# Optimization experiments

Measured on AMD Instinct MI355X. Metric: run time of the kernel, lower is better.

Reference implementation:

```python
import jax, jax.numpy as jnp
import numpy as np

V, E, H, A = 10000, 512, 512, 512  # vocab, embed, hidden, att_odim (== enc dim)
B, T_ENC, L = 32, 1500, 100
BOS, EOS = 1, 2
ATT_H = 512  # attention MLP hidden dim


def setup_inputs() -> dict:
    key = jax.random.key(0)
    ks = jax.random.split(key, 12)
    s = 0.02
    enc_pad = jax.random.normal(ks[0], (B, T_ENC, A), dtype=jnp.float32)
    enc_len = jax.random.randint(ks[1], (B,), T_ENC // 2, T_ENC + 1)
    ys = jax.random.randint(ks[2], (B, L), 3, V)
    return {
        "enc_pad": enc_pad,
        "enc_len": enc_len,
        "ys": ys,
        "emb_table": jax.random.normal(ks[3], (V, E), jnp.float32) * s,
        "W_ih": jax.random.normal(ks[4], (4 * H, E + A), jnp.float32) * s,
        "W_hh": jax.random.normal(ks[5], (4 * H, H), jnp.float32) * s,
        "b_ih": jnp.zeros((4 * H,), jnp.float32),
        "b_hh": jnp.zeros((4 * H,), jnp.float32),
        "W_enc": jax.random.normal(ks[6], (A, ATT_H), jnp.float32) * s,
        "W_dec": jax.random.normal(ks[7], (H, ATT_H), jnp.float32) * s,
        "v_att": jax.random.normal(ks[8], (ATT_H,), jnp.float32) * s,
        "W_out": jax.random.normal(ks[9], (V, H + A), jnp.float32) * s,
        "b_out": jnp.zeros((V,), jnp.float32),
    }


def reference(enc_pad, enc_len, ys, emb_table, W_ih, W_hh, b_ih, b_hh,
              W_enc, W_dec, v_att, W_out, b_out):
    # Teacher-forced decoder (tf_rate=1.0, dropout=0, eval mode, no label smoothing)
    Bz = enc_pad.shape[0]
    bos_col = jnp.full((Bz, 1), BOS, dtype=ys.dtype)
    eos_col = jnp.full((Bz, 1), EOS, dtype=ys.dtype)
    ys_in = jnp.concatenate([bos_col, ys], axis=1)    # [B, L+1]
    ys_out = jnp.concatenate([ys, eos_col], axis=1)   # [B, L+1]
    eys = emb_table[ys_in]                            # [B, L+1, E]

    mask = jnp.arange(enc_pad.shape[1])[None, :] < enc_len[:, None]  # [B, T]
    enc_proj = jnp.einsum('btd,da->bta', enc_pad, W_enc)             # precompute once

    dec_z0 = jnp.zeros((Bz, W_hh.shape[1]), enc_pad.dtype)
    dec_c0 = jnp.zeros((Bz, W_hh.shape[1]), enc_pad.dtype)
    c0 = jnp.zeros((Bz, enc_pad.shape[2]), enc_pad.dtype)

    def step(carry, emb_t):
        dec_z, dec_c, c = carry
        cell_inp = jnp.concatenate([emb_t, c], axis=-1)          # [B, E+A]
        gates = cell_inp @ W_ih.T + b_ih + dec_z @ W_hh.T + b_hh  # [B, 4H]
        i_g, f_g, g_g, o_g = jnp.split(gates, 4, axis=-1)
        dec_c = jax.nn.sigmoid(f_g) * dec_c + jax.nn.sigmoid(i_g) * jnp.tanh(g_g)
        dec_z = jax.nn.sigmoid(o_g) * jnp.tanh(dec_c)
        # additive attention over encoder states, masked by enc_len
        e = jnp.tanh(enc_proj + (dec_z @ W_dec)[:, None, :]) @ v_att  # [B, T]
        e = jnp.where(mask, e, jnp.float32(-1e9))
        w = jax.nn.softmax(e, axis=-1)                                # [B, T]
        c = jnp.einsum('bt,btd->bd', w, enc_pad)                      # [B, A]
        logit = jnp.concatenate([dec_z, c], axis=-1) @ W_out.T + b_out
        return (dec_z, dec_c, c), (logit, w)

    _, (logits_t, ws_t) = jax.lax.scan(step, (dec_z0, dec_c0, c0),
                                       jnp.swapaxes(eys, 0, 1))
    logits = jnp.swapaxes(logits_t, 0, 1)   # [B, L+1, V]
    ws = jnp.swapaxes(ws_t, 0, 1)           # [B, L+1, T]

    log_probs = jax.nn.log_softmax(logits, axis=2)
    prediction = jnp.argmax(logits, axis=-1)
    ys_log_probs = jnp.take_along_axis(log_probs, ys_out[:, :, None], axis=2)[:, :, 0]
    return logits, ys_log_probs, prediction, ws
```

## Files before the change

### kernel.cpp

```cpp
#include <hip/hip_runtime.h>
#include <math.h>

#define BZ   32
#define TENC 1500
#define DD   512
#define VV   10000
#define LL   100
#define SS   101
#define G4   2048
#define KCZ  1024
#define ACH  32
#define NCH  47

#define OUT_LOGITS 0
#define OUT_ENCP   0
#define OUT_PREG   24576000
#define OUT_YSLP   32320000
#define OUT_PRED   32323232
#define OUT_WS     32326464

#define WS_ZA      0
#define WS_CST     3342336
#define WS_LALL    3358720
#define WS_Q       3361952
#define WS_ZERON   3361952

__device__ inline float sigm(float x) { return 1.f / (1.f + __expf(-x)); }
__device__ inline float tanh_fast(float x) {
    x = fminf(15.f, fmaxf(-15.f, x));
    float e = __expf(2.f * x);
    return (e - 1.f) / (e + 1.f);
}

__global__ void zero_kernel(float* ws) {
    size_t i = (size_t)blockIdx.x * 256 + threadIdx.x;
    if (i < WS_ZERON) ws[i] = 0.f;
}

template<int MODE>
__global__ __launch_bounds__(256) void gemm_tile(
    const float* __restrict__ Abase, const float* __restrict__ Bmat,
    const float* __restrict__ bias0, const float* __restrict__ bias1,
    const int* __restrict__ ys, const float* __restrict__ l_all,
    float* __restrict__ Out, int M, int N, int K)
{
    __shared__ float As[16][132];
    __shared__ float Bs[16][132];
    const int tid = threadIdx.x;
    const int row0 = blockIdx.y * 128, n0 = blockIdx.x * 128;

    const int ar = tid >> 1, ah = tid & 1;
    int am = row0 + ar; if (am > M - 1) am = M - 1;
    const float* Arow;
    float linvA = 1.f;
    if (MODE == 0) {
        Arow = Abase + (size_t)am * 512;
    } else if (MODE == 1) {
        int t = am >> 5, b = am & 31;
        int tok = (t == 0) ? 1 : ys[b * LL + t - 1];
        Arow = Abase + (size_t)tok * 512;
    } else {
        Arow = Abase + (size_t)(am + 32) * 1024;
        linvA = 1.f / l_all[am];
    }
    const int bk = tid >> 4, bg = tid & 15;
    const int bn = tid >> 1, bh = tid & 1;
    int bnn = n0 + bn; if (bnn > N - 1) bnn = N - 1;

    const int tx = tid & 15, ty = tid >> 4;
    const int rr = ty * 8, cc = tx * 8;
    float acc[8][8] = {{0.f}};

    for (int k0 = 0; k0 < K; k0 += 16) {
        float4 a0 = *(const float4*)(Arow + k0 + ah * 8);
        float4 a1 = *(const float4*)(Arow + k0 + ah * 8 + 4);
        if (MODE == 2) {
            float sc = (k0 + ah * 8 >= 512) ? linvA : 1.f;
            a0.x *= sc; a0.y *= sc; a0.z *= sc; a0.w *= sc;
            a1.x *= sc; a1.y *= sc; a1.z *= sc; a1.w *= sc;
        }
        As[ah*8+0][ar] = a0.x; As[ah*8+1][ar] = a0.y; As[ah*8+2][ar] = a0.z; As[ah*8+3][ar] = a0.w;
        As[ah*8+4][ar] = a1.x; As[ah*8+5][ar] = a1.y; As[ah*8+6][ar] = a1.z; As[ah*8+7][ar] = a1.w;
        if (MODE == 0) {
            const float* bp = Bmat + (size_t)(k0 + bk) * N + n0 + bg * 8;
            float4 b0 = *(const float4*)(bp);
            float4 b1 = *(const float4*)(bp + 4);
            *(float4*)&Bs[bk][bg * 8]     = b0;
            *(float4*)&Bs[bk][bg * 8 + 4] = b1;
        } else {
            const float* bp = Bmat + (size_t)bnn * 1024 + k0 + bh * 8;
            float4 b0 = *(const float4*)(bp);
            float4 b1 = *(const float4*)(bp + 4);
            Bs[bh*8+0][bn] = b0.x; Bs[bh*8+1][bn] = b0.y; Bs[bh*8+2][bn] = b0.z; Bs[bh*8+3][bn] = b0.w;
            Bs[bh*8+4][bn] = b1.x; Bs[bh*8+5][bn] = b1.y; Bs[bh*8+6][bn] = b1.z; Bs[bh*8+7][bn] = b1.w;
        }
        __syncthreads();
        #pragma unroll
        for (int kk = 0; kk < 16; ++kk) {
            float4 A0 = *(const float4*)&As[kk][rr];
            float4 A1 = *(const float4*)&As[kk][rr + 4];
            float4 B0 = *(const float4*)&Bs[kk][cc];
            float4 B1 = *(const float4*)&Bs[kk][cc + 4];
            float av[8] = {A0.x, A0.y, A0.z, A0.w, A1.x, A1.y, A1.z, A1.w};
            float bv[8] = {B0.x, B0.y, B0.z, B0.w, B1.x, B1.y, B1.z, B1.w};
            #pragma unroll
            for (int i = 0; i < 8; ++i)
                #pragma unroll
                for (int j = 0; j < 8; ++j)
                    acc[i][j] += av[i] * bv[j];
        }
        __syncthreads();
    }
    #pragma unroll
    for (int i = 0; i < 8; ++i) {
        int m = row0 + rr + i;
        if (m >= M) continue;
        size_t orow;
        if (MODE == 2) { int t = m >> 5, b = m & 31; orow = ((size_t)b * SS + t) * (size_t)N; }
        else orow = (size_t)m * N;
        #pragma unroll
        for (int j = 0; j < 8; ++j) {
            int n = n0 + cc + j;
            if (n < N) {
                float v = acc[i][j];
                if (MODE == 1) v += bias0[n] + bias1[n];
                if (MODE == 2) v += bias0[n];
                Out[orow + n] = v;
            }
        }
    }
}

__global__ __launch_bounds__(512) void k_glstm(
    const float* __restrict__ za_t, const float* __restrict__ pre_g_t,
    const float* __restrict__ W_ih, const float* __restrict__ W_hh,
    const float* __restrict__ l_all, int t,
    float* __restrict__ c_state, float* __restrict__ za_n)
{
    __shared__ float red[128];
    const int h = blockIdx.x, tid = threadIdx.x;
    const int wave = tid >> 6, lane = tid & 63;
    const int gl = wave & 3, bh = wave >> 2;
    const int r = gl * 512 + h;
    const float* wz = W_hh + (size_t)r * 512;
    const float* wc = W_ih + (size_t)r * 1024 + 512;
    const float4 wz0 = *(const float4*)(wz + lane * 4);
    const float4 wz1 = *(const float4*)(wz + 256 + lane * 4);
    const float4 wc0 = *(const float4*)(wc + lane * 4);
    const float4 wc1 = *(const float4*)(wc + 256 + lane * 4);

    #pragma unroll 2
    for (int i = 0; i < 16; ++i) {
        const int b = bh * 16 + i;
        const float* zr = za_t + b * KCZ;
        float4 z0 = *(const float4*)(zr + lane * 4);
        float4 z1 = *(const float4*)(zr + 256 + lane * 4);
        float4 c0 = *(const float4*)(zr + 512 + lane * 4);
        float4 c1 = *(const float4*)(zr + 768 + lane * 4);
        float az = z0.x*wz0.x + z0.y*wz0.y + z0.z*wz0.z + z0.w*wz0.w
                 + z1.x*wz1.x + z1.y*wz1.y + z1.z*wz1.z + z1.w*wz1.w;
        float ac = c0.x*wc0.x + c0.y*wc0.y + c0.z*wc0.z + c0.w*wc0.w
                 + c1.x*wc1.x + c1.y*wc1.y + c1.z*wc1.z + c1.w*wc1.w;
        float linv = (t == 0) ? 0.f : 1.f / l_all[(t - 1) * 32 + b];
        float v = az + ac * linv;
        #pragma unroll
        for (int off = 32; off > 0; off >>= 1) v += __shfl_xor(v, off);
        if (lane == 0) red[gl * 32 + b] = v;
    }
    __syncthreads();
    if (tid < 32) {
        const int bb = tid;
        const float* pg = pre_g_t + bb * G4 + h;
        float vi = red[  0 + bb] + pg[0];
        float vf = red[ 32 + bb] + pg[512];
        float vg = red[ 64 + bb] + pg[1024];
        float vo = red[ 96 + bb] + pg[1536];
        float ig = sigm(vi), fg = sigm(vf), gg = tanhf(vg), og = sigm(vo);
        float c = fg * c_state[bb * 512 + h] + ig * gg;
        c_state[bb * 512 + h] = c;
        za_n[bb * KCZ + h] = og * tanhf(c);
    }
}

__global__ __launch_bounds__(256) void k_qproj(const float* __restrict__ za_n,
                                               const float* __restrict__ W_dec,
                                               float* __restrict__ q)
{
    __shared__ float red[256];
    const int tid = threadIdx.x;
    const int j = blockIdx.x * 32 + (tid & 31);
    const int b = blockIdx.y;
    const int k0 = (tid >> 5) * 64;
    const float* z = za_n + b * KCZ + k0;
    const float* wd = W_dec + (size_t)k0 * 512 + j;
    float acc = 0.f;
    #pragma unroll 8
    for (int k = 0; k < 64; k += 4) {
        float4 z4 = *(const float4*)(z + k);
        acc += z4.x * wd[(k + 0) * 512] + z4.y * wd[(k + 1) * 512]
             + z4.z * wd[(k + 2) * 512] + z4.w * wd[(k + 3) * 512];
    }
    red[tid] = acc;
    __syncthreads();
    if (tid < 32) {
        float s = red[tid] + red[tid + 32] + red[tid + 64] + red[tid + 96]
                + red[tid + 128] + red[tid + 160] + red[tid + 192] + red[tid + 224];
        q[b * 512 + blockIdx.x * 32 + tid] = s;
    }
}

__global__ __launch_bounds__(256) void k_att(
    const float* __restrict__ enc_proj, const float* __restrict__ enc_pad,
    const float* __restrict__ q, const float* __restrict__ v_att,
    const int* __restrict__ enc_len,
    float* __restrict__ za_n, float* __restrict__ l_t, float* __restrict__ w_raw)
{
    __shared__ float q_s[512], v_s[512];
    __shared__ float accs[4][512];
    __shared__ float lsum_s[4];
    const int b = blockIdx.y, tc = blockIdx.x, tid = threadIdx.x;
    int len = enc_len[b]; if (len > TENC) len = TENC;
    const int base = tc * ACH;
    int tlim = base + ACH;
    if (tlim > len) tlim = len;
    if (base >= tlim) return;

    for (int i = tid; i < 512; i += 256) { q_s[i] = q[b * 512 + i]; v_s[i] = v_att[i]; }
    __syncthreads();
    const int wave = tid >> 6, lane = tid & 63;
    float a[8] = {0.f, 0.f, 0.f, 0.f, 0.f, 0.f, 0.f, 0.f};
    float lacc = 0.f;
    float qv[8], vv8[8];
    #pragma unroll
    for (int j = 0; j < 8; ++j) { qv[j] = q_s[lane * 8 + j]; vv8[j] = v_s[lane * 8 + j]; }

    for (int tp = base + wave; tp < tlim; tp += 4) {
        const float* ep = enc_proj + ((size_t)b * TENC + tp) * 512 + lane * 8;
        float4 e0 = *(const float4*)(ep);
        float4 e1 = *(const float4*)(ep + 4);
        float s = tanh_fast(e0.x + qv[0]) * vv8[0] + tanh_fast(e0.y + qv[1]) * vv8[1]
                + tanh_fast(e0.z + qv[2]) * vv8[2] + tanh_fast(e0.w + qv[3]) * vv8[3]
                + tanh_fast(e1.x + qv[4]) * vv8[4] + tanh_fast(e1.y + qv[5]) * vv8[5]
                + tanh_fast(e1.z + qv[6]) * vv8[6] + tanh_fast(e1.w + qv[7]) * vv8[7];
        #pragma unroll
        for (int off = 32; off > 0; off >>= 1) s += __shfl_xor(s, off);
        float p = __expf(s - 10.f);
        if (lane == 0) w_raw[(size_t)b * (SS * TENC) + tp] = p;
        lacc += p;
        const float* xp = enc_pad + ((size_t)b * TENC + tp) * 512 + lane * 8;
        float4 x0 = *(const float4*)(xp);
        float4 x1 = *(const float4*)(xp + 4);
        a[0] += p * x0.x; a[1] += p * x0.y; a[2] += p * x0.z; a[3] += p * x0.w;
        a[4] += p * x1.x; a[5] += p * x1.y; a[6] += p * x1.z; a[7] += p * x1.w;
    }
    #pragma unroll
    for (int j = 0; j < 8; ++j) accs[wave][lane * 8 + j] = a[j];
    if (lane == 0) lsum_s[wave] = lacc;
    __syncthreads();
    for (int d = tid; d < 512; d += 256) {
        float s = accs[0][d] + accs[1][d] + accs[2][d] + accs[3][d];
        atomicAdd(&za_n[b * KCZ + 512 + d], s);
    }
    if (tid == 0) atomicAdd(&l_t[b], lsum_s[0] + lsum_s[1] + lsum_s[2] + lsum_s[3]);
}

__global__ __launch_bounds__(256) void k_wnorm(float* __restrict__ wsatt,
                                               const float* __restrict__ l_all,
                                               const int* __restrict__ enc_len)
{
    const int rid = blockIdx.x;
    const int b = rid / SS, t = rid % SS;
    const float linv = 1.f / l_all[t * 32 + b];
    const int len = enc_len[b];
    float* row = wsatt + (size_t)rid * TENC;
    for (int tp = threadIdx.x; tp < TENC; tp += 256)
        row[tp] = (tp < len) ? row[tp] * linv : 0.f;
}

__global__ __launch_bounds__(256) void k_logsm(const float* __restrict__ logits,
                                               const int* __restrict__ ys,
                                               float* __restrict__ ys_lp,
                                               float* __restrict__ pred)
{
    __shared__ float sval[256];
    __shared__ int   sidx[256];
    __shared__ float ssum[256];
    const int bid = blockIdx.x, tid = threadIdx.x;
    const float* row = logits + (size_t)bid * VV;
    float vmax = -3.4e38f; int imax = 0;
    for (int v4 = tid; v4 < VV / 4; v4 += 256) {
        float4 x = *(const float4*)(row + v4 * 4);
        int basei = v4 * 4;
        if (x.x > vmax) { vmax = x.x; imax = basei; }
        if (x.y > vmax) { vmax = x.y; imax = basei + 1; }
        if (x.z > vmax) { vmax = x.z; imax = basei + 2; }
        if (x.w > vmax) { vmax = x.w; imax = basei + 3; }
    }
    sval[tid] = vmax; sidx[tid] = imax;
    __syncthreads();
    for (int s = 128; s > 0; s >>= 1) {
        if (tid < s) {
            float v2 = sval[tid + s]; int i2 = sidx[tid + s];
            if (v2 > sval[tid] || (v2 == sval[tid] && i2 < sidx[tid])) { sval[tid] = v2; sidx[tid] = i2; }
        }
        __syncthreads();
    }
    const float gmax = sval[0];
    float lsum = 0.f;
    for (int v4 = tid; v4 < VV / 4; v4 += 256) {
        float4 x = *(const float4*)(row + v4 * 4);
        lsum += __expf(x.x - gmax) + __expf(x.y - gmax) + __expf(x.z - gmax) + __expf(x.w - gmax);
    }
    ssum[tid] = lsum;
    __syncthreads();
    for (int s = 128; s > 0; s >>= 1) {
        if (tid < s) ssum[tid] += ssum[tid + s];
        __syncthreads();
    }
    if (tid == 0) {
        int b = bid / SS, t = bid % SS;
        int tok = (t < LL) ? ys[b * LL + t] : 2;
        ys_lp[bid] = row[tok] - gmax - logf(ssum[0]);
        pred[bid]  = (float)sidx[0];
    }
}

extern "C" void kernel_launch(void* const* d_in, const int* in_sizes, int n_in,
                              void* d_out, int out_size, void* d_ws, size_t ws_size,
                              hipStream_t stream)
{
    const float* enc_pad = (const float*)d_in[0];
    const int*   enc_len = (const int*)d_in[1];
    const int*   ys      = (const int*)d_in[2];
    const float* emb     = (const float*)d_in[3];
    const float* W_ih    = (const float*)d_in[4];
    const float* W_hh    = (const float*)d_in[5];
    const float* b_ih    = (const float*)d_in[6];
    const float* b_hh    = (const float*)d_in[7];
    const float* W_enc   = (const float*)d_in[8];
    const float* W_dec   = (const float*)d_in[9];
    const float* v_att   = (const float*)d_in[10];
    const float* W_out   = (const float*)d_in[11];
    const float* b_out   = (const float*)d_in[12];

    float* out = (float*)d_out;
    float* enc_proj = out + OUT_ENCP;
    float* pre_g    = out + OUT_PREG;
    float* logits   = out + OUT_LOGITS;
    float* ys_lp    = out + OUT_YSLP;
    float* predo    = out + OUT_PRED;
    float* wsatt    = out + OUT_WS;

    float* ws = (float*)d_ws;
    float* za      = ws + WS_ZA;
    float* c_state = ws + WS_CST;
    float* l_all   = ws + WS_LALL;
    float* qbuf    = ws + WS_Q;

    zero_kernel<<<(WS_ZERON + 255) / 256, 256, 0, stream>>>(ws);
    gemm_tile<0><<<dim3(4, 375), 256, 0, stream>>>(enc_pad, W_enc, nullptr, nullptr, nullptr,
                                                   nullptr, enc_proj, BZ * TENC, 512, 512);
    gemm_tile<1><<<dim3(16, 26), 256, 0, stream>>>(emb, W_ih, b_ih, b_hh, ys,
                                                   nullptr, pre_g, BZ * SS, G4, 512);

    for (int t = 0; t < SS; ++t) {
        float* za_t    = za + (size_t)t * (BZ * KCZ);
        float* za_next = za_t + BZ * KCZ;
        k_glstm<<<512, 512, 0, stream>>>(za_t, pre_g + (size_t)t * (BZ * G4),
                                         W_ih, W_hh, l_all, t, c_state, za_next);
        k_qproj<<<dim3(16, 32), 256, 0, stream>>>(za_next, W_dec, qbuf);
        k_att<<<dim3(NCH, 32), 256, 0, stream>>>(enc_proj, enc_pad, qbuf, v_att, enc_len,
                                                 za_next, l_all + t * 32,
                                                 wsatt + (size_t)t * TENC);
    }

    k_wnorm<<<BZ * SS, 256, 0, stream>>>(wsatt, l_all, enc_len);
    gemm_tile<2><<<dim3(79, 26), 256, 0, stream>>>(za, W_out, b_out, nullptr, nullptr,
                                                   l_all, logits, BZ * SS, VV, 1024);
    k_logsm<<<BZ * SS, 256, 0, stream>>>(logits, ys, ys_lp, predo);
}
```

Before: 6.261 ms.

## Store encoder projection in bf16, restructure LSTM gate matvec, single-pass log-softmax

```diff
diff --git a/kernel.cpp b/kernel.cpp
--- a/kernel.cpp
+++ b/kernel.cpp
@@ -13,7 +13,7 @@
 #define NCH  47
 
 #define OUT_LOGITS 0
-#define OUT_ENCP   0
+#define OUT_ENCPBF 0
 #define OUT_PREG   24576000
 #define OUT_YSLP   32320000
 #define OUT_PRED   32323232
@@ -31,6 +31,13 @@
     float e = __expf(2.f * x);
     return (e - 1.f) / (e + 1.f);
 }
+__device__ inline unsigned short f2bf(float x) {
+    unsigned int u = __float_as_uint(x);
+    u = (u + 0x7FFFu + ((u >> 16) & 1u)) >> 16;
+    return (unsigned short)u;
+}
+__device__ inline float bf_lo(unsigned int u) { return __uint_as_float(u << 16); }
+__device__ inline float bf_hi(unsigned int u) { return __uint_as_float(u & 0xFFFF0000u); }
 
 __global__ void zero_kernel(float* ws) {
     size_t i = (size_t)blockIdx.x * 256 + threadIdx.x;
@@ -111,21 +118,35 @@
         }
         __syncthreads();
     }
-    #pragma unroll
-    for (int i = 0; i < 8; ++i) {
-        int m = row0 + rr + i;
-        if (m >= M) continue;
-        size_t orow;
-        if (MODE == 2) { int t = m >> 5, b = m & 31; orow = ((size_t)b * SS + t) * (size_t)N; }
-        else orow = (size_t)m * N;
-        #pragma unroll
-        for (int j = 0; j < 8; ++j) {
-            int n = n0 + cc + j;
-            if (n < N) {
-                float v = acc[i][j];
-                if (MODE == 1) v += bias0[n] + bias1[n];
-                if (MODE == 2) v += bias0[n];
-                Out[orow + n] = v;
+    if (MODE == 0) {
+        unsigned short* ob = (unsigned short*)Out;
+        #pragma unroll
+        for (int i = 0; i < 8; ++i) {
+            int m = row0 + rr + i;
+            uint4 o;
+            o.x = (unsigned int)f2bf(acc[i][0]) | ((unsigned int)f2bf(acc[i][1]) << 16);
+            o.y = (unsigned int)f2bf(acc[i][2]) | ((unsigned int)f2bf(acc[i][3]) << 16);
+            o.z = (unsigned int)f2bf(acc[i][4]) | ((unsigned int)f2bf(acc[i][5]) << 16);
+            o.w = (unsigned int)f2bf(acc[i][6]) | ((unsigned int)f2bf(acc[i][7]) << 16);
+            *(uint4*)(ob + (size_t)m * 512 + n0 + cc) = o;
+        }
+    } else {
+        #pragma unroll
+        for (int i = 0; i < 8; ++i) {
+            int m = row0 + rr + i;
+            if (m >= M) continue;
+            size_t orow;
+            if (MODE == 2) { int t = m >> 5, b = m & 31; orow = ((size_t)b * SS + t) * (size_t)N; }
+            else orow = (size_t)m * N;
+            #pragma unroll
+            for (int j = 0; j < 8; ++j) {
+                int n = n0 + cc + j;
+                if (n < N) {
+                    float v = acc[i][j];
+                    if (MODE == 1) v += bias0[n] + bias1[n];
+                    if (MODE == 2) v += bias0[n];
+                    Out[orow + n] = v;
+                }
             }
         }
     }
@@ -140,32 +161,36 @@
     __shared__ float red[128];
     const int h = blockIdx.x, tid = threadIdx.x;
     const int wave = tid >> 6, lane = tid & 63;
-    const int gl = wave & 3, bh = wave >> 2;
-    const int r = gl * 512 + h;
-    const float* wz = W_hh + (size_t)r * 512;
-    const float* wc = W_ih + (size_t)r * 1024 + 512;
-    const float4 wz0 = *(const float4*)(wz + lane * 4);
-    const float4 wz1 = *(const float4*)(wz + 256 + lane * 4);
-    const float4 wc0 = *(const float4*)(wc + lane * 4);
-    const float4 wc1 = *(const float4*)(wc + 256 + lane * 4);
-
-    #pragma unroll 2
-    for (int i = 0; i < 16; ++i) {
-        const int b = bh * 16 + i;
+    float4 wz0[4], wz1[4], wc0[4], wc1[4];
+    #pragma unroll
+    for (int g = 0; g < 4; ++g) {
+        const float* wz = W_hh + (size_t)(g * 512 + h) * 512;
+        const float* wc = W_ih + (size_t)(g * 512 + h) * 1024 + 512;
+        wz0[g] = *(const float4*)(wz + lane * 4);
+        wz1[g] = *(const float4*)(wz + 256 + lane * 4);
+        wc0[g] = *(const float4*)(wc + lane * 4);
+        wc1[g] = *(const float4*)(wc + 256 + lane * 4);
+    }
+    #pragma unroll
+    for (int i = 0; i < 4; ++i) {
+        const int b = wave * 4 + i;
         const float* zr = za_t + b * KCZ;
         float4 z0 = *(const float4*)(zr + lane * 4);
         float4 z1 = *(const float4*)(zr + 256 + lane * 4);
         float4 c0 = *(const float4*)(zr + 512 + lane * 4);
         float4 c1 = *(const float4*)(zr + 768 + lane * 4);
-        float az = z0.x*wz0.x + z0.y*wz0.y + z0.z*wz0.z + z0.w*wz0.w
-                 + z1.x*wz1.x + z1.y*wz1.y + z1.z*wz1.z + z1.w*wz1.w;
-        float ac = c0.x*wc0.x + c0.y*wc0.y + c0.z*wc0.z + c0.w*wc0.w
-                 + c1.x*wc1.x + c1.y*wc1.y + c1.z*wc1.z + c1.w*wc1.w;
         float linv = (t == 0) ? 0.f : 1.f / l_all[(t - 1) * 32 + b];
-        float v = az + ac * linv;
-        #pragma unroll
-        for (int off = 32; off > 0; off >>= 1) v += __shfl_xor(v, off);
-        if (lane == 0) red[gl * 32 + b] = v;
+        #pragma unroll
+        for (int g = 0; g < 4; ++g) {
+            float az = z0.x*wz0[g].x + z0.y*wz0[g].y + z0.z*wz0[g].z + z0.w*wz0[g].w
+                     + z1.x*wz1[g].x + z1.y*wz1[g].y + z1.z*wz1[g].z + z1.w*wz1[g].w;
+            float ac = c0.x*wc0[g].x + c0.y*wc0[g].y + c0.z*wc0[g].z + c0.w*wc0[g].w
+                     + c1.x*wc1[g].x + c1.y*wc1[g].y + c1.z*wc1[g].z + c1.w*wc1[g].w;
+            float v = az + ac * linv;
+            #pragma unroll
+            for (int off = 32; off > 0; off >>= 1) v += __shfl_xor(v, off);
+            if (lane == 0) red[g * 32 + b] = v;
+        }
     }
     __syncthreads();
     if (tid < 32) {
@@ -210,7 +235,7 @@
 }
 
 __global__ __launch_bounds__(256) void k_att(
-    const float* __restrict__ enc_proj, const float* __restrict__ enc_pad,
+    const unsigned short* __restrict__ encp_bf, const float* __restrict__ enc_pad,
     const float* __restrict__ q, const float* __restrict__ v_att,
     const int* __restrict__ enc_len,
     float* __restrict__ za_n, float* __restrict__ l_t, float* __restrict__ w_raw)
@@ -235,19 +260,18 @@
     for (int j = 0; j < 8; ++j) { qv[j] = q_s[lane * 8 + j]; vv8[j] = v_s[lane * 8 + j]; }
 
     for (int tp = base + wave; tp < tlim; tp += 4) {
-        const float* ep = enc_proj + ((size_t)b * TENC + tp) * 512 + lane * 8;
-        float4 e0 = *(const float4*)(ep);
-        float4 e1 = *(const float4*)(ep + 4);
-        float s = tanh_fast(e0.x + qv[0]) * vv8[0] + tanh_fast(e0.y + qv[1]) * vv8[1]
-                + tanh_fast(e0.z + qv[2]) * vv8[2] + tanh_fast(e0.w + qv[3]) * vv8[3]
-                + tanh_fast(e1.x + qv[4]) * vv8[4] + tanh_fast(e1.y + qv[5]) * vv8[5]
-                + tanh_fast(e1.z + qv[6]) * vv8[6] + tanh_fast(e1.w + qv[7]) * vv8[7];
+        const size_t roff = ((size_t)b * TENC + tp) * 512 + lane * 8;
+        uint4 E = *(const uint4*)(encp_bf + roff);
+        float s = tanh_fast(bf_lo(E.x) + qv[0]) * vv8[0] + tanh_fast(bf_hi(E.x) + qv[1]) * vv8[1]
+                + tanh_fast(bf_lo(E.y) + qv[2]) * vv8[2] + tanh_fast(bf_hi(E.y) + qv[3]) * vv8[3]
+                + tanh_fast(bf_lo(E.z) + qv[4]) * vv8[4] + tanh_fast(bf_hi(E.z) + qv[5]) * vv8[5]
+                + tanh_fast(bf_lo(E.w) + qv[6]) * vv8[6] + tanh_fast(bf_hi(E.w) + qv[7]) * vv8[7];
         #pragma unroll
         for (int off = 32; off > 0; off >>= 1) s += __shfl_xor(s, off);
         float p = __expf(s - 10.f);
         if (lane == 0) w_raw[(size_t)b * (SS * TENC) + tp] = p;
         lacc += p;
-        const float* xp = enc_pad + ((size_t)b * TENC + tp) * 512 + lane * 8;
+        const float* xp = enc_pad + roff;
         float4 x0 = *(const float4*)(xp);
         float4 x1 = *(const float4*)(xp + 4);
         a[0] += p * x0.x; a[1] += p * x0.y; a[2] += p * x0.z; a[3] += p * x0.w;
@@ -287,40 +311,41 @@
     __shared__ float ssum[256];
     const int bid = blockIdx.x, tid = threadIdx.x;
     const float* row = logits + (size_t)bid * VV;
-    float vmax = -3.4e38f; int imax = 0;
+    float vmax = -3.4e38f; int imax = 0; float lsum = 0.f;
     for (int v4 = tid; v4 < VV / 4; v4 += 256) {
         float4 x = *(const float4*)(row + v4 * 4);
         int basei = v4 * 4;
-        if (x.x > vmax) { vmax = x.x; imax = basei; }
-        if (x.y > vmax) { vmax = x.y; imax = basei + 1; }
-        if (x.z > vmax) { vmax = x.z; imax = basei + 2; }
-        if (x.w > vmax) { vmax = x.w; imax = basei + 3; }
-    }
-    sval[tid] = vmax; sidx[tid] = imax;
+        float e[4] = {x.x, x.y, x.z, x.w};
+        #pragma unroll
+        for (int j = 0; j < 4; ++j) {
+            float v = e[j];
+            if (v > vmax) {
+                lsum = lsum * __expf(vmax - v) + 1.f;
+                vmax = v; imax = basei + j;
+            } else {
+                lsum += __expf(v - vmax);
+            }
+        }
+    }
+    sval[tid] = vmax; sidx[tid] = imax; ssum[tid] = lsum;
     __syncthreads();
     for (int s = 128; s > 0; s >>= 1) {
         if (tid < s) {
-            float v2 = sval[tid + s]; int i2 = sidx[tid + s];
-            if (v2 > sval[tid] || (v2 == sval[tid] && i2 < sidx[tid])) { sval[tid] = v2; sidx[tid] = i2; }
-        }
-        __syncthreads();
-    }
-    const float gmax = sval[0];
-    float lsum = 0.f;
-    for (int v4 = tid; v4 < VV / 4; v4 += 256) {
-        float4 x = *(const float4*)(row + v4 * 4);
-        lsum += __expf(x.x - gmax) + __expf(x.y - gmax) + __expf(x.z - gmax) + __expf(x.w - gmax);
-    }
-    ssum[tid] = lsum;
-    __syncthreads();
-    for (int s = 128; s > 0; s >>= 1) {
-        if (tid < s) ssum[tid] += ssum[tid + s];
+            float v2 = sval[tid + s]; int i2 = sidx[tid + s]; float s2 = ssum[tid + s];
+            float v1 = sval[tid];
+            if (v2 > v1 || (v2 == v1 && i2 < sidx[tid])) {
+                ssum[tid] = s2 + ssum[tid] * __expf(v1 - v2);
+                sval[tid] = v2; sidx[tid] = i2;
+            } else {
+                ssum[tid] = ssum[tid] + s2 * __expf(v2 - v1);
+            }
+        }
         __syncthreads();
     }
     if (tid == 0) {
         int b = bid / SS, t = bid % SS;
         int tok = (t < LL) ? ys[b * LL + t] : 2;
-        ys_lp[bid] = row[tok] - gmax - logf(ssum[0]);
+        ys_lp[bid] = row[tok] - sval[0] - logf(ssum[0]);
         pred[bid]  = (float)sidx[0];
     }
 }
@@ -344,7 +369,7 @@
     const float* b_out   = (const float*)d_in[12];
 
     float* out = (float*)d_out;
-    float* enc_proj = out + OUT_ENCP;
+    unsigned short* encp_bf = (unsigned short*)(out + OUT_ENCPBF);
     float* pre_g    = out + OUT_PREG;
     float* logits   = out + OUT_LOGITS;
     float* ys_lp    = out + OUT_YSLP;
@@ -359,7 +384,7 @@
 
     zero_kernel<<<(WS_ZERON + 255) / 256, 256, 0, stream>>>(ws);
     gemm_tile<0><<<dim3(4, 375), 256, 0, stream>>>(enc_pad, W_enc, nullptr, nullptr, nullptr,
-                                                   nullptr, enc_proj, BZ * TENC, 512, 512);
+                                                   nullptr, (float*)encp_bf, BZ * TENC, 512, 512);
     gemm_tile<1><<<dim3(16, 26), 256, 0, stream>>>(emb, W_ih, b_ih, b_hh, ys,
                                                    nullptr, pre_g, BZ * SS, G4, 512);
 
@@ -369,7 +394,7 @@
         k_glstm<<<512, 512, 0, stream>>>(za_t, pre_g + (size_t)t * (BZ * G4),
                                          W_ih, W_hh, l_all, t, c_state, za_next);
         k_qproj<<<dim3(16, 32), 256, 0, stream>>>(za_next, W_dec, qbuf);
-        k_att<<<dim3(NCH, 32), 256, 0, stream>>>(enc_proj, enc_pad, qbuf, v_att, enc_len,
+        k_att<<<dim3(NCH, 32), 256, 0, stream>>>(encp_bf, enc_pad, qbuf, v_att, enc_len,
                                                  za_next, l_all + t * 32,
                                                  wsatt + (size_t)t * TENC);
     }
```

Result: faster. 5.815 ms (-7.1%).
